# Performance work log

Hardware: AMD Instinct MI355X
Metric: run time of the kernel (lower is better)

Reference implementation:

```python
import jax, jax.numpy as jnp
import numpy as np

NUM_TASKS = 8
NUM_TABLES = 16
HASH = 1_000_000
B = 8192          # bags per table (offsets has B+1 entries, include_last_offset)
L = 20            # average pooling factor
NNZ = B * L       # indices per table


def setup_inputs() -> dict:
    key = jax.random.key(0)
    kw, ki, ko = jax.random.split(key, 3)
    scale = float(np.sqrt(1.0 / HASH))
    # EmbeddingBag weights, uniform(-sqrt(1/h), sqrt(1/h)); embedding_dim=1 folded out.
    weights = jax.random.uniform(kw, (NUM_TASKS, NUM_TABLES, HASH),
                                 minval=-scale, maxval=scale, dtype=jnp.float32)
    indices = jax.random.randint(ki, (NUM_TABLES, NNZ), 0, HASH, dtype=jnp.int32)
    # offsets: sorted partition of [0, NNZ], first=0, last=NNZ (include_last_offset)
    inner = jnp.sort(jax.random.randint(ko, (NUM_TABLES, B - 1), 0, NNZ + 1,
                                        dtype=jnp.int32), axis=1)
    offsets = jnp.concatenate([
        jnp.zeros((NUM_TABLES, 1), jnp.int32),
        inner,
        jnp.full((NUM_TABLES, 1), NNZ, jnp.int32),
    ], axis=1)  # [NUM_TABLES, B+1]
    return {"weights": weights, "offsets": offsets, "indices": indices}


def _segment_ids(off):
    # element j belongs to bag b iff off[b] <= j < off[b+1]
    return jnp.searchsorted(off[1:], jnp.arange(NNZ, dtype=off.dtype), side="right")


def reference(weights, offsets, indices):
    seg = jax.vmap(_segment_ids)(offsets)  # [T, NNZ] bag id per index

    def per_table(w_t, idx, sg):
        # w_t: [N_tasks, H], idx: [NNZ], sg: [NNZ]
        vals = w_t[:, idx]  # gather -> [N_tasks, NNZ]
        return jax.vmap(lambda v: jax.ops.segment_sum(v, sg, num_segments=B))(vals)  # [N_tasks, B]

    # vmap over the table axis -> [T, N_tasks, B]
    pooled = jax.vmap(per_table, in_axes=(1, 0, 0))(weights, indices, seg)
    # match torch: cat per-task [B, T] then view(num_tasks, B, T)
    return jnp.transpose(pooled, (1, 2, 0))  # [N_tasks, B, T]
```

## Files before the change

### kernel.cpp

```cpp
#include <hip/hip_runtime.h>

#define NUM_TASKS 8
#define NUM_TABLES 16
#define HASH 1000000
#define BATCH 8192
#define NNZ (BATCH * 20)
#define OFF_ROW (BATCH + 1)
#define NPASS 16
#define RANGE (HASH / NPASS)
#define CHUNK 640
#define NCHUNK (NNZ / CHUNK)
#define SORT_STRIDE (NNZ + 512)
#define FS_CAP 11264
#define NBIN 3968
#define NPG 4

#define WS_PART  0ull
#define PART_BYTES ((size_t)NPG * NUM_TABLES * NUM_TASKS * BATCH * 4)
#define WS_SORT  PART_BYTES
#define SORT_BYTES ((size_t)NUM_TABLES * SORT_STRIDE * 4)
#define WS_SEG   (WS_SORT + SORT_BYTES)
#define SEG_BYTES ((size_t)NUM_TABLES * NNZ * 4)
#define WS_HIST  (WS_SEG + SEG_BYTES)
#define WS_BB    (WS_HIST + 262144ull)
#define WS_CNTB  (WS_BB + 1024ull)
#define WS_NEED  (WS_CNTB + 1024ull)

__global__ void hist_kernel(const int* __restrict__ indices, const int* __restrict__ offsets,
                            unsigned* __restrict__ hist, unsigned* __restrict__ seg)
{
    int bag_gid = blockIdx.x * 256 + (int)threadIdx.x;
    if (bag_gid < NUM_TABLES * BATCH) {
        int bt = bag_gid >> 13;
        int b  = bag_gid & (BATCH - 1);
        int s  = offsets[bt * OFF_ROW + b];
        int e  = offsets[bt * OFF_ROW + b + 1];
        unsigned* sg = seg + (size_t)bt * NNZ;
        for (int i = s; i < e; ++i) sg[i] = (unsigned)b;
    }

    __shared__ int h[4][NPASS];
    int w = threadIdx.x >> 6, lane = threadIdx.x & 63;
    int g = blockIdx.x * 4 + w;
    int t = g >> 8, chunk = g & 255;
    if (lane < NPASS) h[w][lane] = 0;
    __syncthreads();
    const int* ip = indices + (size_t)t * NNZ + chunk * CHUNK;
    for (int r = 0; r < CHUNK / 64; ++r) {
        int k = ip[r * 64 + lane] / RANGE;
        atomicAdd(&h[w][k], 1);
    }
    __syncthreads();
    if (lane < NPASS) hist[((size_t)t * NPASS + lane) * NCHUNK + chunk] = (unsigned)h[w][lane];
}

__global__ void scan_kernel(unsigned* __restrict__ hist, unsigned* __restrict__ bb, unsigned* __restrict__ cnt)
{
    int t = blockIdx.x, tid = threadIdx.x;
    __shared__ unsigned tot[NPASS];
    if (tid < NPASS) {
        unsigned run = 0;
        unsigned* hp = hist + ((size_t)t * NPASS + tid) * NCHUNK;
        for (int c = 0; c < NCHUNK; ++c) { unsigned v = hp[c]; hp[c] = run; run += v; }
        tot[tid] = run;
        cnt[t * NPASS + tid] = run;
    }
    __syncthreads();
    if (tid == 0) {
        unsigned base = 0;
        for (int k = 0; k < NPASS; ++k) { bb[t * NPASS + k] = base; base += (tot[k] + 31u) & ~31u; }
    }
}

__global__ void scatter_kernel(const int* __restrict__ indices, const unsigned* __restrict__ seg,
                               const unsigned* __restrict__ hist, const unsigned* __restrict__ bb,
                               unsigned* __restrict__ sorted)
{
    int w = threadIdx.x >> 6, lane = threadIdx.x & 63;
    int g = blockIdx.x * 4 + w;
    int t = g >> 8, chunk = g & 255;
    unsigned cur = 0;
    if (lane < NPASS)
        cur = bb[t * NPASS + lane] + hist[((size_t)t * NPASS + lane) * NCHUNK + chunk];
    unsigned long long mlt = (1ull << lane) - 1ull;
    const int* ip      = indices + (size_t)t * NNZ;
    const unsigned* sg = seg + (size_t)t * NNZ;
    unsigned* sp       = sorted + (size_t)t * SORT_STRIDE;

    for (int r = 0; r < CHUNK / 64; ++r) {
        int i = chunk * CHUNK + r * 64 + lane;
        int raw = ip[i];
        unsigned lo = sg[i];
        int k   = raw / RANGE;
        int hlo = raw - k * RANGE;
        unsigned pos = 0;
#pragma unroll
        for (int kk = 0; kk < NPASS; ++kk) {
            unsigned long long m = __ballot(k == kk);
            unsigned bc = (unsigned)__shfl((int)cur, kk, 64);
            if (k == kk) pos = bc + (unsigned)__popcll(m & mlt);
            if (lane == kk) cur += (unsigned)__popcll(m);
        }
        sp[pos] = ((unsigned)hlo << 16) | lo;
    }
}

__global__ __launch_bounds__(256)
void finesort_kernel(unsigned* __restrict__ sorted, const unsigned* __restrict__ bb,
                     const unsigned* __restrict__ cnt)
{
    __shared__ unsigned ebuf[FS_CAP];
    __shared__ unsigned hcnt[NBIN];
    __shared__ unsigned tsum[256];
    int tk = blockIdx.x;
    int t = tk >> 4;
    unsigned n = cnt[tk];
    unsigned* sp = sorted + (size_t)t * SORT_STRIDE + bb[tk];
    int tid = threadIdx.x;
    if (n > FS_CAP) return;

    for (int i = tid; i < NBIN; i += 256) hcnt[i] = 0;
    __syncthreads();
    for (unsigned i = tid; i < n; i += 256) {
        unsigned e = sp[i];
        ebuf[i] = e;
        atomicAdd(&hcnt[e >> 20], 1u);
    }
    __syncthreads();
    {
        int base = tid * 16;
        unsigned s = 0;
        if (base < NBIN) {
#pragma unroll
            for (int e = 0; e < 16; ++e) s += hcnt[base + e];
        }
        tsum[tid] = s;
        __syncthreads();
        if (tid == 0) {
            unsigned run = 0;
            for (int j = 0; j < 256; ++j) { unsigned v = tsum[j]; tsum[j] = run; run += v; }
        }
        __syncthreads();
        if (base < NBIN) {
            unsigned run = tsum[tid];
#pragma unroll
            for (int e = 0; e < 16; ++e) { unsigned v = hcnt[base + e]; hcnt[base + e] = run; run += v; }
        }
    }
    __syncthreads();
    for (unsigned i = tid; i < n; i += 256) {
        unsigned e = ebuf[i];
        unsigned pos = atomicAdd(&hcnt[e >> 20], 1u);
        sp[pos] = e;
    }
}

__global__ __launch_bounds__(1024)
void gather_kernel(const float* __restrict__ W, const unsigned* __restrict__ sorted,
                   const unsigned* __restrict__ bb, const unsigned* __restrict__ cnt,
                   float* __restrict__ partial)
{
    __shared__ float accum[BATCH];
    const int bid  = blockIdx.x;
    const int task = bid & 7;
    const int t    = (bid >> 3) & 15;
    const int pg   = bid >> 7;
    const int tid  = threadIdx.x;

    float4* av = (float4*)accum;
    float4 z4 = make_float4(0.f, 0.f, 0.f, 0.f);
    av[tid]        = z4;
    av[tid + 1024] = z4;
    __syncthreads();

    const float* Wbase = W + ((size_t)task * NUM_TABLES + t) * HASH;

#pragma unroll 1
    for (int j = 0; j < NPASS / NPG; ++j) {
        const int p = pg * (NPASS / NPG) + j;
        const unsigned n = cnt[t * NPASS + p];
        const unsigned* ep = sorted + (size_t)t * SORT_STRIDE + bb[t * NPASS + p];
        const float* Wt = Wbase + (size_t)p * RANGE;
        const uint2* ep2 = (const uint2*)ep;
        const unsigned npair = n >> 1;
        for (unsigned i = tid; i < npair; i += 1024) {
            uint2 e = ep2[i];
            float v0 = Wt[e.x >> 16];
            float v1 = Wt[e.y >> 16];
            atomicAdd(&accum[e.x & 0xFFFFu], v0);
            atomicAdd(&accum[e.y & 0xFFFFu], v1);
        }
        if (tid == 0 && (n & 1u)) {
            unsigned e = ep[n - 1];
            atomicAdd(&accum[e & 0xFFFFu], Wt[e >> 16]);
        }
    }
    __syncthreads();

    float4* pp = (float4*)(partial + (((size_t)(pg * NUM_TABLES + t) * NUM_TASKS) + task) * BATCH);
    pp[tid]        = av[tid];
    pp[tid + 1024] = av[tid + 1024];
}

__global__ void reduce_kernel(const float* __restrict__ partial, float* __restrict__ out)
{
    int tid  = blockIdx.x * blockDim.x + threadIdx.x;
    int task = tid >> 13;
    int b    = tid & (BATCH - 1);

    float s[NUM_TABLES];
#pragma unroll
    for (int t = 0; t < NUM_TABLES; ++t) {
        float a = 0.f;
#pragma unroll
        for (int pg = 0; pg < NPG; ++pg)
            a += partial[(((size_t)(pg * NUM_TABLES + t) * NUM_TASKS) + task) * BATCH + b];
        s[t] = a;
    }

    float4* o = (float4*)(out + ((size_t)task * BATCH + b) * NUM_TABLES);
    o[0] = make_float4(s[0],  s[1],  s[2],  s[3]);
    o[1] = make_float4(s[4],  s[5],  s[6],  s[7]);
    o[2] = make_float4(s[8],  s[9],  s[10], s[11]);
    o[3] = make_float4(s[12], s[13], s[14], s[15]);
}

__global__ void pool_fallback_kernel(const float* __restrict__ W, const int* __restrict__ offsets,
                                     const int* __restrict__ indices, float* __restrict__ out)
{
    const int block = blockIdx.x;
    const int t        = block >> 11;
    const int bag_base = (block & 2047) << 2;
    const int wave     = threadIdx.x >> 6;
    const int b        = bag_base + wave;
    const int lane     = threadIdx.x & 63;
    const int task     = lane & 7;
    const int split    = lane >> 3;
    const int start = offsets[t * OFF_ROW + b];
    const int end   = offsets[t * OFF_ROW + b + 1];
    const int*   idxp   = indices + (size_t)t * NNZ;
    const float* Wslice = W + ((size_t)task * NUM_TABLES + t) * (size_t)HASH;
    float acc = 0.0f;
    for (int i = start + split; i < end; i += 8) acc += Wslice[idxp[i]];
    acc += __shfl_xor(acc, 8); acc += __shfl_xor(acc, 16); acc += __shfl_xor(acc, 32);
    if (split == 0) out[((size_t)task * BATCH + b) * NUM_TABLES + t] = acc;
}

extern "C" void kernel_launch(void* const* d_in, const int* in_sizes, int n_in,
                              void* d_out, int out_size, void* d_ws, size_t ws_size,
                              hipStream_t stream) {
    const float* W       = (const float*)d_in[0];
    const int*   offsets = (const int*)d_in[1];
    const int*   indices = (const int*)d_in[2];
    float*       out     = (float*)d_out;

    if (ws_size < WS_NEED) {
        pool_fallback_kernel<<<NUM_TABLES * 2048, 256, 0, stream>>>(W, offsets, indices, out);
        return;
    }

    float*    partial = (float*)((char*)d_ws + WS_PART);
    unsigned* sorted  = (unsigned*)((char*)d_ws + WS_SORT);
    unsigned* seg     = (unsigned*)((char*)d_ws + WS_SEG);
    unsigned* hist    = (unsigned*)((char*)d_ws + WS_HIST);
    unsigned* bb      = (unsigned*)((char*)d_ws + WS_BB);
    unsigned* cntb    = (unsigned*)((char*)d_ws + WS_CNTB);

    hist_kernel<<<(NUM_TABLES * NCHUNK) / 4, 256, 0, stream>>>(indices, offsets, hist, seg);
    scan_kernel<<<NUM_TABLES, 64, 0, stream>>>(hist, bb, cntb);
    scatter_kernel<<<(NUM_TABLES * NCHUNK) / 4, 256, 0, stream>>>(indices, seg, hist, bb, sorted);
    finesort_kernel<<<NUM_TABLES * NPASS, 256, 0, stream>>>(sorted, bb, cntb);
    gather_kernel<<<NPG * NUM_TABLES * NUM_TASKS, 1024, 0, stream>>>(W, sorted, bb, cntb, partial);
    reduce_kernel<<<(NUM_TASKS * BATCH) / 256, 256, 0, stream>>>(partial, out);
}
```

Baseline: 192.7 us.

## Stage weight tiles in LDS per fine bin and gather from shared memory

Finesort now writes its per-bin prefix offsets to a workspace array, and the gather kernel walks those fine bins one wave at a time. Each wave loads a contiguous 64-float4 tile of weights into LDS, then resolves the indices in that bin range with LDS reads instead of random global loads. This turns scattered global gathers into coalesced streaming reads of the weight rows, and adds per-chunk waits, extra LDS traffic and possible load imbalance across waves. Hist and scatter also interleave tables across block IDs. The finesort early-exit capacity guard is dropped, with a slightly larger buffer instead.

```diff
diff --git a/kernel.cpp b/kernel.cpp
--- a/kernel.cpp
+++ b/kernel.cpp
@@ -11,9 +11,11 @@
 #define CHUNK 640
 #define NCHUNK (NNZ / CHUNK)
 #define SORT_STRIDE (NNZ + 512)
-#define FS_CAP 11264
-#define NBIN 3968
+#define FS_CAP 11776
+#define NBIN_T 3907
+#define NBIN_PAD 3968
 #define NPG 4
+#define LPW 245
 
 #define WS_PART  0ull
 #define PART_BYTES ((size_t)NPG * NUM_TABLES * NUM_TASKS * BATCH * 4)
@@ -24,7 +26,9 @@
 #define WS_HIST  (WS_SEG + SEG_BYTES)
 #define WS_BB    (WS_HIST + 262144ull)
 #define WS_CNTB  (WS_BB + 1024ull)
-#define WS_NEED  (WS_CNTB + 1024ull)
+#define WS_LRP   (WS_CNTB + 1024ull)
+#define LRP_BYTES ((size_t)NUM_TABLES * NPASS * (NBIN_T + 1) * 4)
+#define WS_NEED  (WS_LRP + LRP_BYTES)
 
 __global__ void hist_kernel(const int* __restrict__ indices, const int* __restrict__ offsets,
                             unsigned* __restrict__ hist, unsigned* __restrict__ seg)
@@ -41,8 +45,9 @@
 
     __shared__ int h[4][NPASS];
     int w = threadIdx.x >> 6, lane = threadIdx.x & 63;
-    int g = blockIdx.x * 4 + w;
-    int t = g >> 8, chunk = g & 255;
+    int bid = blockIdx.x;
+    int t     = bid & 15;
+    int chunk = (bid >> 4) * 4 + w;
     if (lane < NPASS) h[w][lane] = 0;
     __syncthreads();
     const int* ip = indices + (size_t)t * NNZ + chunk * CHUNK;
@@ -77,8 +82,9 @@
                                unsigned* __restrict__ sorted)
 {
     int w = threadIdx.x >> 6, lane = threadIdx.x & 63;
-    int g = blockIdx.x * 4 + w;
-    int t = g >> 8, chunk = g & 255;
+    int bid = blockIdx.x;
+    int t     = bid & 15;
+    int chunk = (bid >> 4) * 4 + w;
     unsigned cur = 0;
     if (lane < NPASS)
         cur = bb[t * NPASS + lane] + hist[((size_t)t * NPASS + lane) * NCHUNK + chunk];
@@ -107,19 +113,19 @@
 
 __global__ __launch_bounds__(256)
 void finesort_kernel(unsigned* __restrict__ sorted, const unsigned* __restrict__ bb,
-                     const unsigned* __restrict__ cnt)
+                     const unsigned* __restrict__ cnt, unsigned* __restrict__ lrp)
 {
     __shared__ unsigned ebuf[FS_CAP];
-    __shared__ unsigned hcnt[NBIN];
+    __shared__ unsigned hcnt[NBIN_PAD];
     __shared__ unsigned tsum[256];
     int tk = blockIdx.x;
     int t = tk >> 4;
     unsigned n = cnt[tk];
     unsigned* sp = sorted + (size_t)t * SORT_STRIDE + bb[tk];
+    unsigned* lr = lrp + (size_t)tk * (NBIN_T + 1);
     int tid = threadIdx.x;
-    if (n > FS_CAP) return;
-
-    for (int i = tid; i < NBIN; i += 256) hcnt[i] = 0;
+
+    for (int i = tid; i < NBIN_PAD; i += 256) hcnt[i] = 0;
     __syncthreads();
     for (unsigned i = tid; i < n; i += 256) {
         unsigned e = sp[i];
@@ -130,7 +136,7 @@
     {
         int base = tid * 16;
         unsigned s = 0;
-        if (base < NBIN) {
+        if (base < NBIN_PAD) {
 #pragma unroll
             for (int e = 0; e < 16; ++e) s += hcnt[base + e];
         }
@@ -141,12 +147,14 @@
             for (int j = 0; j < 256; ++j) { unsigned v = tsum[j]; tsum[j] = run; run += v; }
         }
         __syncthreads();
-        if (base < NBIN) {
+        if (base < NBIN_PAD) {
             unsigned run = tsum[tid];
 #pragma unroll
             for (int e = 0; e < 16; ++e) { unsigned v = hcnt[base + e]; hcnt[base + e] = run; run += v; }
         }
     }
+    __syncthreads();
+    for (int i = tid; i <= NBIN_T; i += 256) lr[i] = hcnt[i];
     __syncthreads();
     for (unsigned i = tid; i < n; i += 256) {
         unsigned e = ebuf[i];
@@ -157,15 +165,18 @@
 
 __global__ __launch_bounds__(1024)
 void gather_kernel(const float* __restrict__ W, const unsigned* __restrict__ sorted,
-                   const unsigned* __restrict__ bb, const unsigned* __restrict__ cnt,
+                   const unsigned* __restrict__ bb, const unsigned* __restrict__ lrp,
                    float* __restrict__ partial)
 {
-    __shared__ float accum[BATCH];
+    __shared__ float  accum[BATCH];
+    __shared__ float4 tile4[16][64];
     const int bid  = blockIdx.x;
     const int task = bid & 7;
     const int t    = (bid >> 3) & 15;
     const int pg   = bid >> 7;
     const int tid  = threadIdx.x;
+    const int wv   = tid >> 6;
+    const int lane = tid & 63;
 
     float4* av = (float4*)accum;
     float4 z4 = make_float4(0.f, 0.f, 0.f, 0.f);
@@ -174,25 +185,31 @@
     __syncthreads();
 
     const float* Wbase = W + ((size_t)task * NUM_TABLES + t) * HASH;
+    const int w0 = wv * LPW;
+    const int w1 = min(NBIN_T, w0 + LPW);
+    float* tilef = (float*)tile4[wv];
 
 #pragma unroll 1
     for (int j = 0; j < NPASS / NPG; ++j) {
         const int p = pg * (NPASS / NPG) + j;
-        const unsigned n = cnt[t * NPASS + p];
         const unsigned* ep = sorted + (size_t)t * SORT_STRIDE + bb[t * NPASS + p];
-        const float* Wt = Wbase + (size_t)p * RANGE;
-        const uint2* ep2 = (const uint2*)ep;
-        const unsigned npair = n >> 1;
-        for (unsigned i = tid; i < npair; i += 1024) {
-            uint2 e = ep2[i];
-            float v0 = Wt[e.x >> 16];
-            float v1 = Wt[e.y >> 16];
-            atomicAdd(&accum[e.x & 0xFFFFu], v0);
-            atomicAdd(&accum[e.y & 0xFFFFu], v1);
-        }
-        if (tid == 0 && (n & 1u)) {
-            unsigned e = ep[n - 1];
-            atomicAdd(&accum[e & 0xFFFFu], Wt[e >> 16]);
+        const unsigned* lr = lrp + (size_t)(t * NPASS + p) * (NBIN_T + 1);
+        const float4* Wt4 = (const float4*)(Wbase + (size_t)p * RANGE);
+
+#pragma unroll 1
+        for (int c = w0; c < w1; c += 16) {
+            const int cs = min(16, w1 - c);
+            asm volatile("s_waitcnt lgkmcnt(0)" ::: "memory");
+            const int f = c * 4 + lane;
+            if (lane < cs * 4 && f < RANGE / 4) tile4[wv][lane] = Wt4[f];
+            const unsigned e0 = lr[c];
+            const unsigned e1 = lr[c + cs];
+            asm volatile("s_waitcnt lgkmcnt(0)" ::: "memory");
+            __builtin_amdgcn_sched_barrier(0);
+            for (unsigned i = e0 + lane; i < e1; i += 64) {
+                unsigned e = ep[i];
+                atomicAdd(&accum[e & 0xFFFFu], tilef[(e >> 16) - c * 16]);
+            }
         }
     }
     __syncthreads();
@@ -265,11 +282,12 @@
     unsigned* hist    = (unsigned*)((char*)d_ws + WS_HIST);
     unsigned* bb      = (unsigned*)((char*)d_ws + WS_BB);
     unsigned* cntb    = (unsigned*)((char*)d_ws + WS_CNTB);
+    unsigned* lrp     = (unsigned*)((char*)d_ws + WS_LRP);
 
     hist_kernel<<<(NUM_TABLES * NCHUNK) / 4, 256, 0, stream>>>(indices, offsets, hist, seg);
     scan_kernel<<<NUM_TABLES, 64, 0, stream>>>(hist, bb, cntb);
     scatter_kernel<<<(NUM_TABLES * NCHUNK) / 4, 256, 0, stream>>>(indices, seg, hist, bb, sorted);
-    finesort_kernel<<<NUM_TABLES * NPASS, 256, 0, stream>>>(sorted, bb, cntb);
-    gather_kernel<<<NPG * NUM_TABLES * NUM_TASKS, 1024, 0, stream>>>(W, sorted, bb, cntb, partial);
+    finesort_kernel<<<NUM_TABLES * NPASS, 256, 0, stream>>>(sorted, bb, cntb, lrp);
+    gather_kernel<<<NPG * NUM_TABLES * NUM_TASKS, 1024, 0, stream>>>(W, sorted, bb, lrp, partial);
     reduce_kernel<<<(NUM_TASKS * BATCH) / 256, 256, 0, stream>>>(partial, out);
 }
```

Measured after the change: 227.3 us. +18.0%, slower.
